# Kernel tuning notes

Hardware: AMD Instinct MI355X
Metric: run time of the kernel (lower is better)

## Reference

```python
import jax, jax.numpy as jnp
import numpy as np

OBS_LEN = 20
PRED_LEN = 30
H = 64          # h_dim
E = 16          # embedding_dim
B = 32768       # num_agents
IN_FEAT = OBS_LEN * 2  # 40
EPS = 1e-5


def layer_norm(x, g, b):
    m = jnp.mean(x, axis=-1, keepdims=True)
    v = jnp.mean((x - m) ** 2, axis=-1, keepdims=True)
    return (x - m) / jnp.sqrt(v + EPS) * g + b


def setup_inputs() -> dict:
    key = jax.random.key(0)
    ks = jax.random.split(key, 16)
    s = 0.1
    return {
        "traj_abs": jax.random.normal(ks[0], (OBS_LEN, B, 2), jnp.float32),
        "traj_rel": jax.random.normal(ks[1], (OBS_LEN, B, 2), jnp.float32),
        "decoder_h": jax.random.normal(ks[2], (1, B, H), jnp.float32),
        # LSTM params (PyTorch gate order: i, f, g, o)
        "W_ih": jax.random.normal(ks[3], (4 * H, E), jnp.float32) * s,
        "W_hh": jax.random.normal(ks[4], (4 * H, H), jnp.float32) * s,
        "b_ih": jax.random.normal(ks[5], (4 * H,), jnp.float32) * s,
        "b_hh": jax.random.normal(ks[6], (4 * H,), jnp.float32) * s,
        # spatial_embedding: Linear(40 -> 16)
        "emb_W": jax.random.normal(ks[7], (E, IN_FEAT), jnp.float32) * s,
        "emb_b": jax.random.normal(ks[8], (E,), jnp.float32) * s,
        # hidden2pos: Linear(64 -> 2)
        "h2p_W": jax.random.normal(ks[9], (2, H), jnp.float32) * s,
        "h2p_b": jax.random.normal(ks[10], (2,), jnp.float32) * s,
        # LayerNorms
        "ln1_g": jnp.ones((IN_FEAT,), jnp.float32),
        "ln1_b": jnp.zeros((IN_FEAT,), jnp.float32),
        "ln2_g": jnp.ones((H,), jnp.float32),
        "ln2_b": jnp.zeros((H,), jnp.float32),
    }


def reference(traj_abs, traj_rel, decoder_h, W_ih, W_hh, b_ih, b_hh,
              emb_W, emb_b, h2p_W, h2p_b, ln1_g, ln1_b, ln2_g, ln2_b):
    # use_rel_disp=False branch; D=1, num_layers=1 => LSTM is a single cell.
    h0 = decoder_h[0]                      # (B, H)
    c0 = jnp.zeros_like(h0)

    def step(carry, _):
        traj, h, c = carry
        # faithful to torch .view(num_agents, -1): raw row-major reshape (20,B,2)->(B,40)
        x = jax.nn.leaky_relu(
            layer_norm(traj.reshape(B, IN_FEAT), ln1_g, ln1_b) @ emb_W.T + emb_b
        )  # (B, E)
        gates = x @ W_ih.T + b_ih + h @ W_hh.T + b_hh   # (B, 4H)
        i, f, g, o = jnp.split(gates, 4, axis=-1)
        c = jax.nn.sigmoid(f) * c + jax.nn.sigmoid(i) * jnp.tanh(g)
        h = jax.nn.sigmoid(o) * jnp.tanh(c)
        pos = layer_norm(h, ln2_g, ln2_b) @ h2p_W.T + h2p_b  # (B, 2)
        traj = jnp.concatenate([traj[1:], pos[None]], axis=0)  # roll -1 on dim 0, set last
        return (traj, h, c), pos

    _, pred = jax.lax.scan(step, (traj_abs, h0, c0), None, length=PRED_LEN)
    return pred  # (PRED_LEN, B, 2)
```

## Files before the change

### kernel.cpp

```cpp
#include <hip/hip_runtime.h>
#include <hip/hip_bf16.h>

#define NAGENTS 32768
#define SLAB    65536
#define SPLIT   1310720
#define SPLIT4  327680
#define PRED    30
#define IN_F    40
#define LN_EPS  1e-5f
#define APB     128
#define NBLK    (NAGENTS/APB)
#define BTH     1024
#define XSTRIDE 104
#define RSTR    72

typedef short bf16x8 __attribute__((ext_vector_type(8)));
typedef short bf16x4 __attribute__((ext_vector_type(4)));
typedef float f32x4  __attribute__((ext_vector_type(4)));

#define C_SGW  0
#define C_BW   16
#define C_G2   32
#define C_SG2  160
#define C_B2   162
#define C_BIAS 164
#define C_TOT  420

__device__ __forceinline__ float frcp(float x){ return __builtin_amdgcn_rcpf(x); }
__device__ __forceinline__ float fsigmoid(float x){ return frcp(1.f + __expf(-x)); }
__device__ __forceinline__ float ftanh(float x){
    float t = __expf(-2.f*fabsf(x));
    float r = (1.f - t) * frcp(1.f + t);
    return copysignf(r, x);
}
__device__ __forceinline__ float lrelu(float x){ return x > 0.f ? x : 0.01f*x; }
__device__ __forceinline__ short f2bf(float x){
    unsigned u = __float_as_uint(x);
    return (short)((u + 0x7FFFu + ((u>>16)&1u)) >> 16);
}
__device__ __forceinline__ float bf2f(short s){
    return __uint_as_float(((unsigned)(unsigned short)s) << 16);
}
__device__ __forceinline__ unsigned pk_bf16(float a, float b){
    __hip_bfloat162 h = __float22bfloat162_rn(float2{a, b});
    return *reinterpret_cast<unsigned*>(&h);
}

__global__ __launch_bounds__(BTH, 4)
void persist_kernel(const float* __restrict__ traj,
                    float* __restrict__ out,
                    const float* __restrict__ dec_h,
                    const float* __restrict__ W_ih, const float* __restrict__ W_hh,
                    const float* __restrict__ b_ih, const float* __restrict__ b_hh,
                    const float* __restrict__ emb_W, const float* __restrict__ emb_b,
                    const float* __restrict__ h2p_W, const float* __restrict__ h2p_b,
                    const float* __restrict__ ln1_g, const float* __restrict__ ln1_b,
                    const float* __restrict__ ln2_g, const float* __restrict__ ln2_b,
                    int* __restrict__ flags)
{
    __shared__ short Rs[APB*RSTR];
    __shared__ short Xs[APB*XSTRIDE];
    __shared__ float Ds[APB*16];
    __shared__ float St[APB*2];
    __shared__ float cst[C_TOT];

    const int tid  = threadIdx.x;
    const int bid  = blockIdx.x;
    const int a0   = bid * APB;
    const int l    = tid & 63;
    const int wv   = tid >> 6;
    const int gang = wv >> 2;
    const int wvin = wv & 3;
    const int cl   = l & 15;
    const int kb   = l >> 4;
    const int nh   = wvin*16 + cl;

    if (tid < 16) {
        int e = tid;
        float s = 0.f, b = 0.f;
        for (int f = 0; f < IN_F; ++f) {
            float wf = emb_W[e*40 + f];
            s += ln1_g[f] * wf;
            b += ln1_b[f] * wf;
        }
        cst[C_SGW + e] = s;
        cst[C_BW + e]  = b + emb_b[e];
    }
    if (tid < 128) {
        int k = tid >> 1, d = tid & 1;
        cst[C_G2 + tid] = ln2_g[k] * h2p_W[d*64 + k];
    }
    if (tid < 2) {
        int d = tid;
        float s = 0.f, b = 0.f;
        for (int k = 0; k < 64; ++k) {
            float wf = h2p_W[d*64 + k];
            s += ln2_g[k] * wf;
            b += ln2_b[k] * wf;
        }
        cst[C_SG2 + d] = s;
        cst[C_B2 + d]  = b + h2p_b[d];
    }
    if (tid >= 256 && tid < 512) cst[C_BIAS + tid - 256] = b_ih[tid-256] + b_hh[tid-256];

    bf16x8 bw[4][3];
#pragma unroll
    for (int g = 0; g < 4; ++g)
#pragma unroll
        for (int ks = 0; ks < 3; ++ks) {
            int n = g*64 + nh;
            bf16x8 v;
#pragma unroll
            for (int j = 0; j < 8; ++j) {
                int k = ks*32 + kb*8 + j;
                float f = 0.f;
                if (k < 16)      f = W_ih[n*16 + k];
                else if (k < 80) f = W_hh[n*64 + (k-16)];
                v[j] = f2bf(f);
            }
            bw[g][ks] = v;
        }

    bf16x8 ew[2];
#pragma unroll
    for (int ks = 0; ks < 2; ++ks) {
        bf16x8 v;
#pragma unroll
        for (int j = 0; j < 8; ++j) {
            int k = ks*32 + kb*8 + j;
            float f = (k < IN_F) ? ln1_g[k] * emb_W[cl*40 + k] : 0.f;
            v[j] = f2bf(f);
        }
        ew[ks] = v;
    }

    for (int i = tid; i < APB*16; i += BTH) {
        int a = i >> 4, q = i & 15;
        float4 hv = ((const float4*)dec_h)[(a0 + a)*16 + q];
        uint2 pv{ pk_bf16(hv.x, hv.y), pk_bf16(hv.z, hv.w) };
        *(uint2*)&Xs[a*XSTRIDE + 16 + q*4] = pv;
    }
    if (tid < APB*2) {
        int a = tid >> 1, hf = tid & 1;
        *(bf16x8*)&Xs[a*XSTRIDE + 80 + hf*8] = bf16x8{0,0,0,0,0,0,0,0};
    }
    for (int i = tid; i < APB*3; i += BTH) {
        int a = i / 3, seg = i - a*3;
        *(bf16x8*)&Rs[a*RSTR + 40 + seg*8] = bf16x8{0,0,0,0,0,0,0,0};
    }

    float cs[2][4];
#pragma unroll
    for (int mt = 0; mt < 2; ++mt)
#pragma unroll
        for (int r = 0; r < 4; ++r) cs[mt][r] = 0.f;

    __syncthreads();

    for (int s = 0; s < PRED; ++s) {
        {
            const long Ob = (long)s*SLAB + (long)a0*IN_F - SPLIT;
            const long Oe = Ob + APB*IN_F;
            if (Oe > 0) {
                long o0 = Ob < 0 ? 0 : Ob;
                int i0 = (int)(o0 >> 8);
                int i1 = (int)((Oe - 1) >> 8);
                for (int i = i0 + tid; i <= i1; i += BTH) {
                    int t = i >> 8, p = i & 255;
                    while (__hip_atomic_load(&flags[p], __ATOMIC_ACQUIRE,
                                             __HIP_MEMORY_SCOPE_AGENT) < t + 1)
                        __builtin_amdgcn_s_sleep(1);
                }
            }
        }
        __syncthreads();

        {
            const int Gb4 = s*(SLAB/4) + bid*(APB*IN_F/4);
            for (int i = tid; i < APB*IN_F/4; i += BTH) {
                int a = i / 10, f4 = i - a*10;
                int G4 = Gb4 + i;
                float4 v = (G4 < SPLIT4) ? ((const float4*)traj)[G4]
                                         : ((const float4*)out)[G4 - SPLIT4];
                uint2 pv{ pk_bf16(v.x, v.y), pk_bf16(v.z, v.w) };
                *(uint2*)&Rs[a*RSTR + f4*4] = pv;
            }
        }
        __syncthreads();

        if (wv < 8) {
            f32x4 dacc = f32x4{0.f, 0.f, 0.f, 0.f};
            const short* base = &Rs[(wv*16 + cl)*RSTR + kb*8];
            bf16x8 a0f = *(const bf16x8*)(base);
            bf16x8 a1f = *(const bf16x8*)(base + 32);
            dacc = __builtin_amdgcn_mfma_f32_16x16x32_bf16(a0f, ew[0], dacc, 0, 0, 0);
            dacc = __builtin_amdgcn_mfma_f32_16x16x32_bf16(a1f, ew[1], dacc, 0, 0, 0);
#pragma unroll
            for (int r = 0; r < 4; ++r)
                Ds[(wv*16 + kb*4 + r)*16 + cl] = dacc[r];
        } else {
            int t2 = tid - 512;
            int a = t2 >> 2, p = t2 & 3;
            const bf16x8* rp = (const bf16x8*)&Rs[a*RSTR + p*16];
            bf16x8 v0 = rp[0], v1 = rp[1];
            float s1 = 0.f, s2 = 0.f;
#pragma unroll
            for (int j = 0; j < 8; ++j) {
                float f0 = bf2f(v0[j]), f1 = bf2f(v1[j]);
                s1 += f0 + f1; s2 += f0*f0 + f1*f1;
            }
            s1 += __shfl_xor(s1, 1, 64); s2 += __shfl_xor(s2, 1, 64);
            s1 += __shfl_xor(s1, 2, 64); s2 += __shfl_xor(s2, 2, 64);
            if (p == 0) {
                float m = s1 * (1.f/IN_F);
                St[a*2]   = m;
                St[a*2+1] = rsqrtf(s2*(1.f/IN_F) - m*m + LN_EPS);
            }
        }
        __syncthreads();

        {
            int a = tid >> 3, p = tid & 7, e0 = p*2;
            float m = St[a*2], inv = St[a*2+1];
            float D0 = Ds[a*16 + e0], D1 = Ds[a*16 + e0 + 1];
            float x0 = inv*(D0 - m*cst[C_SGW+e0  ]) + cst[C_BW+e0  ];
            float x1 = inv*(D1 - m*cst[C_SGW+e0+1]) + cst[C_BW+e0+1];
            unsigned pv = pk_bf16(lrelu(x0), lrelu(x1));
            *(unsigned*)&Xs[a*XSTRIDE + e0] = pv;
        }
        __syncthreads();

        f32x4 acc[2][4];
#pragma unroll
        for (int g = 0; g < 4; ++g) {
            float bb = cst[C_BIAS + g*64 + nh];
            acc[0][g] = f32x4{bb, bb, bb, bb};
            acc[1][g] = f32x4{bb, bb, bb, bb};
        }
#pragma unroll
        for (int mt = 0; mt < 2; ++mt) {
            const short* base = &Xs[(gang*32 + mt*16 + cl)*XSTRIDE + kb*8];
            bf16x8 af0 = *(const bf16x8*)(base);
            bf16x8 af1 = *(const bf16x8*)(base + 32);
            bf16x8 af2 = *(const bf16x8*)(base + 64);
#pragma unroll
            for (int g = 0; g < 4; ++g) {
                acc[mt][g] = __builtin_amdgcn_mfma_f32_16x16x32_bf16(af0, bw[g][0], acc[mt][g], 0, 0, 0);
                acc[mt][g] = __builtin_amdgcn_mfma_f32_16x16x32_bf16(af1, bw[g][1], acc[mt][g], 0, 0, 0);
                acc[mt][g] = __builtin_amdgcn_mfma_f32_16x16x32_bf16(af2, bw[g][2], acc[mt][g], 0, 0, 0);
            }
        }
        __syncthreads();

#pragma unroll
        for (int mt = 0; mt < 2; ++mt) {
            int abase = gang*32 + mt*16 + kb*4;
#pragma unroll
            for (int r = 0; r < 4; ++r) {
                float cn = fsigmoid(acc[mt][1][r]) * cs[mt][r]
                         + fsigmoid(acc[mt][0][r]) * ftanh(acc[mt][2][r]);
                float hn = fsigmoid(acc[mt][3][r]) * ftanh(cn);
                cs[mt][r] = cn;
                Xs[(abase + r)*XSTRIDE + 16 + nh] = f2bf(hn);
            }
        }
        __syncthreads();

        {
            int a = tid >> 3, p = tid & 7;
            bf16x8 hv = *(const bf16x8*)&Xs[a*XSTRIDE + 16 + p*8];
            float s1 = 0.f, s2 = 0.f, d0 = 0.f, d1 = 0.f;
#pragma unroll
            for (int j = 0; j < 8; ++j) {
                float f = bf2f(hv[j]);
                float2 gw = *(const float2*)&cst[C_G2 + (p*8 + j)*2];
                s1 += f; s2 += f*f;
                d0 += f*gw.x; d1 += f*gw.y;
            }
#pragma unroll
            for (int mk = 1; mk < 8; mk <<= 1) {
                s1 += __shfl_xor(s1, mk, 64);
                s2 += __shfl_xor(s2, mk, 64);
                d0 += __shfl_xor(d0, mk, 64);
                d1 += __shfl_xor(d1, mk, 64);
            }
            if (p < 2) {
                float m   = s1 * (1.f/64);
                float inv = rsqrtf(s2*(1.f/64) - m*m + LN_EPS);
                float dd  = (p == 0) ? d0 : d1;
                float val = inv*(dd - m*cst[C_SG2+p]) + cst[C_B2+p];
                __hip_atomic_store(&out[s*SLAB + (a0 + a)*2 + p], val,
                                   __ATOMIC_RELAXED, __HIP_MEMORY_SCOPE_AGENT);
            }
        }

        if (s != PRED-1) {
            __syncthreads();
            if (tid == 0)
                __hip_atomic_store(&flags[bid], s+1, __ATOMIC_RELAXED,
                                   __HIP_MEMORY_SCOPE_AGENT);
        }
    }
}

extern "C" void kernel_launch(void* const* d_in, const int* in_sizes, int n_in,
                              void* d_out, int out_size, void* d_ws, size_t ws_size,
                              hipStream_t stream) {
    const float* traj  = (const float*)d_in[0];
    const float* dec_h = (const float*)d_in[2];
    const float* W_ih  = (const float*)d_in[3];
    const float* W_hh  = (const float*)d_in[4];
    const float* b_ih  = (const float*)d_in[5];
    const float* b_hh  = (const float*)d_in[6];
    const float* emb_W = (const float*)d_in[7];
    const float* emb_b = (const float*)d_in[8];
    const float* h2p_W = (const float*)d_in[9];
    const float* h2p_b = (const float*)d_in[10];
    const float* ln1_g = (const float*)d_in[11];
    const float* ln1_b = (const float*)d_in[12];
    const float* ln2_g = (const float*)d_in[13];
    const float* ln2_b = (const float*)d_in[14];
    float* out = (float*)d_out;
    int*   flg = (int*)d_ws;

    persist_kernel<<<NBLK, BTH, 0, stream>>>(
        traj, out, dec_h, W_ih, W_hh, b_ih, b_hh, emb_W, emb_b,
        h2p_W, h2p_b, ln1_g, ln1_b, ln2_g, ln2_b, flg);
}
```

Measured before the change: 315.3 us.

## Overlap recurrent h-GEMM with trajectory load and fuse input LayerNorm into MFMA wave

Reorders the Xs layout so the hidden state comes first, letting the W_hh part of the gate GEMM run while the trajectory window is loaded. The input LayerNorm statistics are computed inside the embedding MFMA waves via shuffles, which removes the Ds/St shared buffers and two barriers per step. Gate weights and biases are pre-scaled by -log2e (-2log2e for g) so the activations use exp2 with combined reciprocals. Block IDs are also remapped to change scheduling order. The cost is more intricate register and lane mapping, and a small change in numerics from the combined reciprocals.

```diff
diff --git a/kernel.cpp b/kernel.cpp
--- a/kernel.cpp
+++ b/kernel.cpp
@@ -13,9 +13,9 @@
 #define BTH     1024
 #define XSTRIDE 104
 #define RSTR    72
+#define LOG2E   1.44269504088896f
 
 typedef short bf16x8 __attribute__((ext_vector_type(8)));
-typedef short bf16x4 __attribute__((ext_vector_type(4)));
 typedef float f32x4  __attribute__((ext_vector_type(4)));
 
 #define C_SGW  0
@@ -27,12 +27,7 @@
 #define C_TOT  420
 
 __device__ __forceinline__ float frcp(float x){ return __builtin_amdgcn_rcpf(x); }
-__device__ __forceinline__ float fsigmoid(float x){ return frcp(1.f + __expf(-x)); }
-__device__ __forceinline__ float ftanh(float x){
-    float t = __expf(-2.f*fabsf(x));
-    float r = (1.f - t) * frcp(1.f + t);
-    return copysignf(r, x);
-}
+__device__ __forceinline__ float fexp2(float x){ return __builtin_amdgcn_exp2f(x); }
 __device__ __forceinline__ float lrelu(float x){ return x > 0.f ? x : 0.01f*x; }
 __device__ __forceinline__ short f2bf(float x){
     unsigned u = __float_as_uint(x);
@@ -60,12 +55,10 @@
 {
     __shared__ short Rs[APB*RSTR];
     __shared__ short Xs[APB*XSTRIDE];
-    __shared__ float Ds[APB*16];
-    __shared__ float St[APB*2];
     __shared__ float cst[C_TOT];
 
     const int tid  = threadIdx.x;
-    const int bid  = blockIdx.x;
+    const int bid  = ((blockIdx.x & 7) << 5) | (blockIdx.x >> 3);
     const int a0   = bid * APB;
     const int l    = tid & 63;
     const int wv   = tid >> 6;
@@ -101,11 +94,16 @@
         cst[C_SG2 + d] = s;
         cst[C_B2 + d]  = b + h2p_b[d];
     }
-    if (tid >= 256 && tid < 512) cst[C_BIAS + tid - 256] = b_ih[tid-256] + b_hh[tid-256];
+    if (tid >= 256 && tid < 512) {
+        int idx = tid - 256;
+        float sc = ((idx >> 6) == 2) ? (-2.f*LOG2E) : (-LOG2E);
+        cst[C_BIAS + idx] = (b_ih[idx] + b_hh[idx]) * sc;
+    }
 
     bf16x8 bw[4][3];
 #pragma unroll
-    for (int g = 0; g < 4; ++g)
+    for (int g = 0; g < 4; ++g) {
+        float sc = (g == 2) ? (-2.f*LOG2E) : (-LOG2E);
 #pragma unroll
         for (int ks = 0; ks < 3; ++ks) {
             int n = g*64 + nh;
@@ -114,12 +112,13 @@
             for (int j = 0; j < 8; ++j) {
                 int k = ks*32 + kb*8 + j;
                 float f = 0.f;
-                if (k < 16)      f = W_ih[n*16 + k];
-                else if (k < 80) f = W_hh[n*64 + (k-16)];
-                v[j] = f2bf(f);
+                if (k < 64)      f = W_hh[n*64 + k];
+                else if (k < 80) f = W_ih[n*16 + (k-64)];
+                v[j] = f2bf(f * sc);
             }
             bw[g][ks] = v;
         }
+    }
 
     bf16x8 ew[2];
 #pragma unroll
@@ -138,14 +137,14 @@
         int a = i >> 4, q = i & 15;
         float4 hv = ((const float4*)dec_h)[(a0 + a)*16 + q];
         uint2 pv{ pk_bf16(hv.x, hv.y), pk_bf16(hv.z, hv.w) };
-        *(uint2*)&Xs[a*XSTRIDE + 16 + q*4] = pv;
+        *(uint2*)&Xs[a*XSTRIDE + q*4] = pv;
     }
     if (tid < APB*2) {
         int a = tid >> 1, hf = tid & 1;
         *(bf16x8*)&Xs[a*XSTRIDE + 80 + hf*8] = bf16x8{0,0,0,0,0,0,0,0};
     }
-    for (int i = tid; i < APB*3; i += BTH) {
-        int a = i / 3, seg = i - a*3;
+    if (tid < APB*3) {
+        int a = tid / 3, seg = tid - a*3;
         *(bf16x8*)&Rs[a*RSTR + 40 + seg*8] = bf16x8{0,0,0,0,0,0,0,0};
     }
 
@@ -175,60 +174,17 @@
         }
         __syncthreads();
 
-        {
-            const int Gb4 = s*(SLAB/4) + bid*(APB*IN_F/4);
-            for (int i = tid; i < APB*IN_F/4; i += BTH) {
-                int a = i / 10, f4 = i - a*10;
-                int G4 = Gb4 + i;
-                float4 v = (G4 < SPLIT4) ? ((const float4*)traj)[G4]
-                                         : ((const float4*)out)[G4 - SPLIT4];
-                uint2 pv{ pk_bf16(v.x, v.y), pk_bf16(v.z, v.w) };
-                *(uint2*)&Rs[a*RSTR + f4*4] = pv;
-            }
-        }
-        __syncthreads();
-
-        if (wv < 8) {
-            f32x4 dacc = f32x4{0.f, 0.f, 0.f, 0.f};
-            const short* base = &Rs[(wv*16 + cl)*RSTR + kb*8];
-            bf16x8 a0f = *(const bf16x8*)(base);
-            bf16x8 a1f = *(const bf16x8*)(base + 32);
-            dacc = __builtin_amdgcn_mfma_f32_16x16x32_bf16(a0f, ew[0], dacc, 0, 0, 0);
-            dacc = __builtin_amdgcn_mfma_f32_16x16x32_bf16(a1f, ew[1], dacc, 0, 0, 0);
-#pragma unroll
-            for (int r = 0; r < 4; ++r)
-                Ds[(wv*16 + kb*4 + r)*16 + cl] = dacc[r];
-        } else {
-            int t2 = tid - 512;
-            int a = t2 >> 2, p = t2 & 3;
-            const bf16x8* rp = (const bf16x8*)&Rs[a*RSTR + p*16];
-            bf16x8 v0 = rp[0], v1 = rp[1];
-            float s1 = 0.f, s2 = 0.f;
-#pragma unroll
-            for (int j = 0; j < 8; ++j) {
-                float f0 = bf2f(v0[j]), f1 = bf2f(v1[j]);
-                s1 += f0 + f1; s2 += f0*f0 + f1*f1;
-            }
-            s1 += __shfl_xor(s1, 1, 64); s2 += __shfl_xor(s2, 1, 64);
-            s1 += __shfl_xor(s1, 2, 64); s2 += __shfl_xor(s2, 2, 64);
-            if (p == 0) {
-                float m = s1 * (1.f/IN_F);
-                St[a*2]   = m;
-                St[a*2+1] = rsqrtf(s2*(1.f/IN_F) - m*m + LN_EPS);
-            }
-        }
-        __syncthreads();
-
-        {
-            int a = tid >> 3, p = tid & 7, e0 = p*2;
-            float m = St[a*2], inv = St[a*2+1];
-            float D0 = Ds[a*16 + e0], D1 = Ds[a*16 + e0 + 1];
-            float x0 = inv*(D0 - m*cst[C_SGW+e0  ]) + cst[C_BW+e0  ];
-            float x1 = inv*(D1 - m*cst[C_SGW+e0+1]) + cst[C_BW+e0+1];
-            unsigned pv = pk_bf16(lrelu(x0), lrelu(x1));
-            *(unsigned*)&Xs[a*XSTRIDE + e0] = pv;
-        }
-        __syncthreads();
+        const int Gb4 = s*(SLAB/4) + bid*(APB*IN_F/4);
+        const int G0 = Gb4 + tid;
+        float4 v0 = (G0 < SPLIT4) ? ((const float4*)traj)[G0]
+                                  : ((const float4*)out)[G0 - SPLIT4];
+        float4 v1;
+        const bool extra = (tid < (APB*IN_F/4 - BTH));
+        if (extra) {
+            int G1 = G0 + BTH;
+            v1 = (G1 < SPLIT4) ? ((const float4*)traj)[G1]
+                               : ((const float4*)out)[G1 - SPLIT4];
+        }
 
         f32x4 acc[2][4];
 #pragma unroll
@@ -239,36 +195,102 @@
         }
 #pragma unroll
         for (int mt = 0; mt < 2; ++mt) {
-            const short* base = &Xs[(gang*32 + mt*16 + cl)*XSTRIDE + kb*8];
-            bf16x8 af0 = *(const bf16x8*)(base);
-            bf16x8 af1 = *(const bf16x8*)(base + 32);
-            bf16x8 af2 = *(const bf16x8*)(base + 64);
+            const short* hb = &Xs[(gang*32 + mt*16 + cl)*XSTRIDE + kb*8];
+            bf16x8 hf0 = *(const bf16x8*)(hb);
+            bf16x8 hf1 = *(const bf16x8*)(hb + 32);
 #pragma unroll
             for (int g = 0; g < 4; ++g) {
-                acc[mt][g] = __builtin_amdgcn_mfma_f32_16x16x32_bf16(af0, bw[g][0], acc[mt][g], 0, 0, 0);
-                acc[mt][g] = __builtin_amdgcn_mfma_f32_16x16x32_bf16(af1, bw[g][1], acc[mt][g], 0, 0, 0);
-                acc[mt][g] = __builtin_amdgcn_mfma_f32_16x16x32_bf16(af2, bw[g][2], acc[mt][g], 0, 0, 0);
+                acc[mt][g] = __builtin_amdgcn_mfma_f32_16x16x32_bf16(hf0, bw[g][0], acc[mt][g], 0, 0, 0);
+                acc[mt][g] = __builtin_amdgcn_mfma_f32_16x16x32_bf16(hf1, bw[g][1], acc[mt][g], 0, 0, 0);
+            }
+        }
+
+        {
+            int a = tid / 10, f4 = tid - a*10;
+            uint2 w{ pk_bf16(v0.x, v0.y), pk_bf16(v0.z, v0.w) };
+            *(uint2*)&Rs[a*RSTR + f4*4] = w;
+            if (extra) {
+                int i2 = tid + BTH, a2 = i2 / 10, f42 = i2 - a2*10;
+                uint2 w2{ pk_bf16(v1.x, v1.y), pk_bf16(v1.z, v1.w) };
+                *(uint2*)&Rs[a2*RSTR + f42*4] = w2;
             }
         }
         __syncthreads();
 
+        if (wv < 8) {
+            const short* base = &Rs[(wv*16 + cl)*RSTR + kb*8];
+            bf16x8 a0f = *(const bf16x8*)(base);
+            bf16x8 a1f = *(const bf16x8*)(base + 32);
+            f32x4 dacc = f32x4{0.f, 0.f, 0.f, 0.f};
+            dacc = __builtin_amdgcn_mfma_f32_16x16x32_bf16(a0f, ew[0], dacc, 0, 0, 0);
+            dacc = __builtin_amdgcn_mfma_f32_16x16x32_bf16(a1f, ew[1], dacc, 0, 0, 0);
+            float s1 = 0.f, s2 = 0.f;
+#pragma unroll
+            for (int j = 0; j < 8; ++j) {
+                float f0 = bf2f(a0f[j]), f1 = bf2f(a1f[j]);
+                s1 += f0 + f1; s2 += f0*f0 + f1*f1;
+            }
+            s1 += __shfl_xor(s1, 16, 64); s2 += __shfl_xor(s2, 16, 64);
+            s1 += __shfl_xor(s1, 32, 64); s2 += __shfl_xor(s2, 32, 64);
+            float m  = s1 * (1.f/IN_F);
+            float iv = rsqrtf(s2*(1.f/IN_F) - m*m + LN_EPS);
+            float sgw = cst[C_SGW + cl], bwc = cst[C_BW + cl];
+            float xr[4];
+#pragma unroll
+            for (int r = 0; r < 4; ++r) {
+                float mm = __shfl(m,  kb*4 + r, 64);
+                float ii = __shfl(iv, kb*4 + r, 64);
+                xr[r] = lrelu(ii*(dacc[r] - mm*sgw) + bwc);
+            }
+            unsigned u01 = pk_bf16(xr[0], xr[1]);
+            unsigned u23 = pk_bf16(xr[2], xr[3]);
+            int rb = (wv*16 + kb*4)*XSTRIDE + 64 + cl;
+            Xs[rb]             = (short)(u01 & 0xFFFFu);
+            Xs[rb + XSTRIDE]   = (short)(u01 >> 16);
+            Xs[rb + 2*XSTRIDE] = (short)(u23 & 0xFFFFu);
+            Xs[rb + 3*XSTRIDE] = (short)(u23 >> 16);
+        }
+        __syncthreads();
+
+#pragma unroll
+        for (int mt = 0; mt < 2; ++mt) {
+            bf16x8 xf = *(const bf16x8*)&Xs[(gang*32 + mt*16 + cl)*XSTRIDE + 64 + kb*8];
+#pragma unroll
+            for (int g = 0; g < 4; ++g)
+                acc[mt][g] = __builtin_amdgcn_mfma_f32_16x16x32_bf16(xf, bw[g][2], acc[mt][g], 0, 0, 0);
+        }
 #pragma unroll
         for (int mt = 0; mt < 2; ++mt) {
             int abase = gang*32 + mt*16 + kb*4;
+            float hn[4];
 #pragma unroll
             for (int r = 0; r < 4; ++r) {
-                float cn = fsigmoid(acc[mt][1][r]) * cs[mt][r]
-                         + fsigmoid(acc[mt][0][r]) * ftanh(acc[mt][2][r]);
-                float hn = fsigmoid(acc[mt][3][r]) * ftanh(cn);
-                cs[mt][r] = cn;
-                Xs[(abase + r)*XSTRIDE + 16 + nh] = f2bf(hn);
-            }
+                float ei = fexp2(acc[mt][0][r]);
+                float ef = fexp2(acc[mt][1][r]);
+                float eg = fexp2(acc[mt][2][r]);
+                float eo = fexp2(acc[mt][3][r]);
+                float r1   = frcp((1.f+ei)*(1.f+eg));
+                float tgsi = (1.f-eg)*r1;
+                float sf   = frcp(1.f+ef);
+                float cn   = fmaf(cs[mt][r], sf, tgsi);
+                float t2   = fexp2(cn * (-2.f*LOG2E));
+                float r2   = frcp((1.f+eo)*(1.f+t2));
+                hn[r]      = (1.f-t2)*r2;
+                cs[mt][r]  = cn;
+            }
+            unsigned u01 = pk_bf16(hn[0], hn[1]);
+            unsigned u23 = pk_bf16(hn[2], hn[3]);
+            int hb = abase*XSTRIDE + nh;
+            Xs[hb]             = (short)(u01 & 0xFFFFu);
+            Xs[hb + XSTRIDE]   = (short)(u01 >> 16);
+            Xs[hb + 2*XSTRIDE] = (short)(u23 & 0xFFFFu);
+            Xs[hb + 3*XSTRIDE] = (short)(u23 >> 16);
         }
         __syncthreads();
 
         {
             int a = tid >> 3, p = tid & 7;
-            bf16x8 hv = *(const bf16x8*)&Xs[a*XSTRIDE + 16 + p*8];
+            bf16x8 hv = *(const bf16x8*)&Xs[a*XSTRIDE + p*8];
             float s1 = 0.f, s2 = 0.f, d0 = 0.f, d1 = 0.f;
 #pragma unroll
             for (int j = 0; j < 8; ++j) {
```

New measurement: 448.7 us. +42.3%, slower.
